# Kernel tuning notes

Hardware: AMD Instinct MI355X
Metric: run time of the kernel (lower is better)

Reference implementation:

```python
import jax, jax.numpy as jnp
import numpy as np


def setup_inputs() -> dict:
    key = jax.random.key(0)
    k1, k2 = jax.random.split(key)
    B, N, M, D = 32, 2048, 2048, 3
    x = jax.random.normal(k1, (B, N, D), dtype=jnp.float32)
    y = jax.random.normal(k2, (B, M, D), dtype=jnp.float32)
    return {"x": x, "y": y}


def reference(x, y):
    # x: [B, N, D], y: [B, M, D]
    # dist[b, m, n] = ||x[b, n] - y[b, m]||^2  -> [B, M, N]
    diff = x[:, None, :, :] - y[:, :, None, :]          # [B, M, N, D]
    dist = jnp.sum(diff * diff, axis=-1)                # [B, M, N]
    # min over M (axis 1): for each x-point, nearest y-point; mean over N
    row = jnp.mean(jnp.min(dist, axis=1), axis=-1)      # [B]
    # min over N (axis 2): for each y-point, nearest x-point; mean over M
    col = jnp.mean(jnp.min(dist, axis=2), axis=-1)      # [B]
    # per-batch max of the two directed means, then mean over batch
    return jnp.mean(jnp.maximum(row, col))
```

## Files before the change

### kernel.cpp

```cpp
#include <hip/hip_runtime.h>


#define BATCH   32
#define NPTS    2048
#define THREADS 128
#define QPT     16
#define TCH     64
#define TC      (NPTS / TCH)
#define NROWB   (BATCH * 8)
#define NCOLB   BATCH

__global__ __launch_bounds__(THREADS, 4) void chamfer_min(
    const float* __restrict__ x, const float* __restrict__ y,
    float* __restrict__ part    ,
    float* __restrict__ colmin  )
{
    __shared__ float4 t4[TC];
    __shared__ float colLds[THREADS][TC + 1];
    __shared__ float cmPart[4][TC + 1];

    const int blk   = blockIdx.x;
    const int b     = blk >> 6;
    const int chunk = blk & 63;

    const float* qp = x + (size_t)b * NPTS * 3;
    const float* tp = y + (size_t)b * NPTS * 3;

    if (threadIdx.x < TC) {
        int jj = chunk * TC + threadIdx.x;
        float ty0 = tp[3 * jj + 0];
        float ty1 = tp[3 * jj + 1];
        float ty2 = tp[3 * jj + 2];
        t4[threadIdx.x] = make_float4(ty0, ty1, ty2,
                                      0.5f * (ty0 * ty0 + ty1 * ty1 + ty2 * ty2));
    }

    float nqx[QPT], nqy[QPT], nqz[QPT], hx[QPT], mn[QPT];
#pragma unroll
    for (int k = 0; k < QPT; ++k) {
        int qi = threadIdx.x + k * THREADS;
        float qx = qp[3 * qi + 0];
        float qy = qp[3 * qi + 1];
        float qz = qp[3 * qi + 2];
        nqx[k] = -qx;
        nqy[k] = -qy;
        nqz[k] = -qz;
        hx[k]  = 0.5f * (qx * qx + qy * qy + qz * qz);
        mn[k]  = 3.4e38f;
    }
    __syncthreads();

#pragma unroll 2
    for (int j = 0; j < TC; j += 2) {
        float4 a = t4[j];
        float4 c4 = t4[j + 1];
        float colA = 3.4e38f, colB = 3.4e38f;
#pragma unroll
        for (int k = 0; k < QPT; k += 2) {
            float Wa0 = a.w  + hx[k],     Wb0 = c4.w + hx[k];
            float Wa1 = a.w  + hx[k + 1], Wb1 = c4.w + hx[k + 1];
            float s0 = fmaf(nqz[k], a.z, fmaf(nqy[k], a.y, fmaf(nqx[k], a.x, Wa0)));
            float s1 = fmaf(nqz[k], c4.z, fmaf(nqy[k], c4.y, fmaf(nqx[k], c4.x, Wb0)));
            float t0 = fmaf(nqz[k+1], a.z, fmaf(nqy[k+1], a.y, fmaf(nqx[k+1], a.x, Wa1)));
            float t1 = fmaf(nqz[k+1], c4.z, fmaf(nqy[k+1], c4.y, fmaf(nqx[k+1], c4.x, Wb1)));
            mn[k]     = fminf(fminf(mn[k], s0), s1);
            mn[k + 1] = fminf(fminf(mn[k + 1], t0), t1);
            colA = fminf(fminf(colA, s0), t0);
            colB = fminf(fminf(colB, s1), t1);
        }
        colLds[threadIdx.x][j]     = colA;
        colLds[threadIdx.x][j + 1] = colB;
    }
    __syncthreads();

    {
        const int g = threadIdx.x >> 5;
        const int j = threadIdx.x & 31;
        float cp = 3.4e38f;
#pragma unroll
        for (int i = 0; i < 32; ++i)
            cp = fminf(cp, colLds[g * 32 + i][j]);
        cmPart[g][j] = cp;
    }
    __syncthreads();
    if (threadIdx.x < TC) {
        const int j = threadIdx.x;
        float cm = fminf(fminf(cmPart[0][j], cmPart[1][j]),
                         fminf(cmPart[2][j], cmPart[3][j]));
        colmin[(size_t)b * NPTS + chunk * TC + j] = cm;
    }

    float* pbase = part + ((size_t)b * TCH + chunk) * NPTS;
#pragma unroll
    for (int k = 0; k < QPT; ++k)
        pbase[threadIdx.x + k * THREADS] = mn[k];
}

#define CTHREADS 256

__global__ __launch_bounds__(CTHREADS) void chamfer_combine(
    const float* __restrict__ part,
    const float* __restrict__ colmin,
    float* __restrict__ blocksums )
{
    __shared__ float wsum[CTHREADS / 64];

    const int blk = blockIdx.x;
    float d;

    if (blk < NROWB) {
        const int b  = blk >> 3;
        const int qc = blk & 7;
        const int qi = qc * CTHREADS + threadIdx.x;
        const float* p = part + (size_t)b * TCH * NPTS + qi;
        float mn = p[0];
#pragma unroll
        for (int c = 1; c < TCH; ++c)
            mn = fminf(mn, p[(size_t)c * NPTS]);
        d = 2.0f * mn;
    } else {
        const int b = blk - NROWB;
        const float* p = colmin + (size_t)b * NPTS;
        float s = 0.0f;
#pragma unroll
        for (int i = 0; i < 8; ++i)
            s += p[threadIdx.x + i * CTHREADS];
        d = 2.0f * s;
    }

    for (int off = 32; off > 0; off >>= 1)
        d += __shfl_down(d, off);
    if ((threadIdx.x & 63) == 0) wsum[threadIdx.x >> 6] = d;
    __syncthreads();
    if (threadIdx.x == 0)
        blocksums[blk] = wsum[0] + wsum[1] + wsum[2] + wsum[3];
}

__global__ void chamfer_finalize(const float* __restrict__ blocksums,
                                 float* __restrict__ out)
{
    const int lane = threadIdx.x;
    float v = 0.0f;
    if (lane < BATCH) {
        float rs = 0.0f;
#pragma unroll
        for (int i = 0; i < 8; ++i)
            rs += blocksums[lane * 8 + i];
        float cs = blocksums[NROWB + lane];
        v = fmaxf(rs, cs) * (1.0f / NPTS);
    }
    for (int off = 32; off > 0; off >>= 1)
        v += __shfl_down(v, off);
    if (lane == 0) out[0] = v * (1.0f / BATCH);
}

extern "C" void kernel_launch(void* const* d_in, const int* in_sizes, int n_in,
                              void* d_out, int out_size, void* d_ws, size_t ws_size,
                              hipStream_t stream) {
    const float* x = (const float*)d_in[0];
    const float* y = (const float*)d_in[1];
    float* out = (float*)d_out;

    float* part      = (float*)d_ws;
    float* colmin    = part + (size_t)BATCH * TCH * NPTS;
    float* blocksums = colmin + (size_t)BATCH * NPTS;

    chamfer_min<<<BATCH * TCH, THREADS, 0, stream>>>(x, y, part, colmin);
    chamfer_combine<<<NROWB + NCOLB, CTHREADS, 0, stream>>>(part, colmin, blocksums);
    chamfer_finalize<<<1, 64, 0, stream>>>(blocksums, out);
}
```

Before: 84.21 us.

## Enlarge per-block target chunk and cut partial-min buffer with grouped column reduction

Each block now runs 256 threads with 8 queries per thread and covers 128 target points instead of 32, so the batch is split into 16 chunks rather than 64. This shrinks the per-chunk row-min partial buffer written by the first kernel and re-read by the combine kernel to a quarter of its former size. To keep the column-min shared-memory tile small, targets are processed in groups of 32, each followed by a block-level column reduction. The cost is more barriers per block, fewer blocks in the grid and less ILP per thread, since each thread now holds fewer query points.

```diff
diff --git a/kernel.cpp b/kernel.cpp
--- a/kernel.cpp
+++ b/kernel.cpp
@@ -3,25 +3,27 @@
 
 #define BATCH   32
 #define NPTS    2048
-#define THREADS 128
-#define QPT     16
-#define TCH     64
+#define THREADS 256
+#define QPT     8
+#define TCH     16
 #define TC      (NPTS / TCH)
+#define GRP     32
+#define NGRP    (TC / GRP)
 #define NROWB   (BATCH * 8)
 #define NCOLB   BATCH
 
-__global__ __launch_bounds__(THREADS, 4) void chamfer_min(
+__global__ __launch_bounds__(THREADS) void chamfer_min(
     const float* __restrict__ x, const float* __restrict__ y,
     float* __restrict__ part    ,
     float* __restrict__ colmin  )
 {
     __shared__ float4 t4[TC];
-    __shared__ float colLds[THREADS][TC + 1];
-    __shared__ float cmPart[4][TC + 1];
+    __shared__ float colLds[THREADS][GRP + 1];
+    __shared__ float cmPart[8][GRP + 1];
 
     const int blk   = blockIdx.x;
-    const int b     = blk >> 6;
-    const int chunk = blk & 63;
+    const int b     = blk >> 4;
+    const int chunk = blk & 15;
 
     const float* qp = x + (size_t)b * NPTS * 3;
     const float* tp = y + (size_t)b * NPTS * 3;
@@ -50,44 +52,50 @@
     }
     __syncthreads();
 
+#pragma unroll 1
+    for (int g = 0; g < NGRP; ++g) {
+        const float4* tg = &t4[g * GRP];
 #pragma unroll 2
-    for (int j = 0; j < TC; j += 2) {
-        float4 a = t4[j];
-        float4 c4 = t4[j + 1];
-        float colA = 3.4e38f, colB = 3.4e38f;
+        for (int j = 0; j < GRP; j += 2) {
+            float4 a  = tg[j];
+            float4 c4 = tg[j + 1];
+            float colA = 3.4e38f, colB = 3.4e38f;
 #pragma unroll
-        for (int k = 0; k < QPT; k += 2) {
-            float Wa0 = a.w  + hx[k],     Wb0 = c4.w + hx[k];
-            float Wa1 = a.w  + hx[k + 1], Wb1 = c4.w + hx[k + 1];
-            float s0 = fmaf(nqz[k], a.z, fmaf(nqy[k], a.y, fmaf(nqx[k], a.x, Wa0)));
-            float s1 = fmaf(nqz[k], c4.z, fmaf(nqy[k], c4.y, fmaf(nqx[k], c4.x, Wb0)));
-            float t0 = fmaf(nqz[k+1], a.z, fmaf(nqy[k+1], a.y, fmaf(nqx[k+1], a.x, Wa1)));
-            float t1 = fmaf(nqz[k+1], c4.z, fmaf(nqy[k+1], c4.y, fmaf(nqx[k+1], c4.x, Wb1)));
-            mn[k]     = fminf(fminf(mn[k], s0), s1);
-            mn[k + 1] = fminf(fminf(mn[k + 1], t0), t1);
-            colA = fminf(fminf(colA, s0), t0);
-            colB = fminf(fminf(colB, s1), t1);
+            for (int k = 0; k < QPT; k += 2) {
+                float Wa0 = a.w  + hx[k],     Wb0 = c4.w + hx[k];
+                float Wa1 = a.w  + hx[k + 1], Wb1 = c4.w + hx[k + 1];
+                float s0 = fmaf(nqz[k], a.z, fmaf(nqy[k], a.y, fmaf(nqx[k], a.x, Wa0)));
+                float s1 = fmaf(nqz[k], c4.z, fmaf(nqy[k], c4.y, fmaf(nqx[k], c4.x, Wb0)));
+                float t0 = fmaf(nqz[k+1], a.z, fmaf(nqy[k+1], a.y, fmaf(nqx[k+1], a.x, Wa1)));
+                float t1 = fmaf(nqz[k+1], c4.z, fmaf(nqy[k+1], c4.y, fmaf(nqx[k+1], c4.x, Wb1)));
+                mn[k]     = fminf(fminf(mn[k], s0), s1);
+                mn[k + 1] = fminf(fminf(mn[k + 1], t0), t1);
+                colA = fminf(fminf(colA, s0), t0);
+                colB = fminf(fminf(colB, s1), t1);
+            }
+            colLds[threadIdx.x][j]     = colA;
+            colLds[threadIdx.x][j + 1] = colB;
         }
-        colLds[threadIdx.x][j]     = colA;
-        colLds[threadIdx.x][j + 1] = colB;
-    }
-    __syncthreads();
+        __syncthreads();
 
-    {
-        const int g = threadIdx.x >> 5;
-        const int j = threadIdx.x & 31;
-        float cp = 3.4e38f;
+        {
+            const int rg = threadIdx.x >> 5;
+            const int t  = threadIdx.x & 31;
+            float cp = 3.4e38f;
 #pragma unroll
-        for (int i = 0; i < 32; ++i)
-            cp = fminf(cp, colLds[g * 32 + i][j]);
-        cmPart[g][j] = cp;
-    }
-    __syncthreads();
-    if (threadIdx.x < TC) {
-        const int j = threadIdx.x;
-        float cm = fminf(fminf(cmPart[0][j], cmPart[1][j]),
-                         fminf(cmPart[2][j], cmPart[3][j]));
-        colmin[(size_t)b * NPTS + chunk * TC + j] = cm;
+            for (int i = 0; i < 32; ++i)
+                cp = fminf(cp, colLds[rg * 32 + i][t]);
+            cmPart[rg][t] = cp;
+        }
+        __syncthreads();
+        if (threadIdx.x < GRP) {
+            const int t = threadIdx.x;
+            float cm = fminf(
+                fminf(fminf(cmPart[0][t], cmPart[1][t]), fminf(cmPart[2][t], cmPart[3][t])),
+                fminf(fminf(cmPart[4][t], cmPart[5][t]), fminf(cmPart[6][t], cmPart[7][t])));
+            colmin[(size_t)b * NPTS + chunk * TC + g * GRP + t] = cm;
+        }
+        __syncthreads();
     }
 
     float* pbase = part + ((size_t)b * TCH + chunk) * NPTS;
```

New measurement: 78.64 us. 6.6% less time.
